# Kernel tuning notes

Measured on AMD Instinct MI355X. Metric: run time of the kernel, lower is better.

## Reference

```python
import jax, jax.numpy as jnp
import numpy as np

N_NODES = 100000
N_EDGES = 1600000
IN_DIM = 512
HID_DIM = 64
N_CLASSES = 10
N_GRAPHS = 64


def setup_inputs() -> dict:
    key = jax.random.key(0)
    ks = jax.random.split(key, 8)
    x = jax.random.normal(ks[0], (N_NODES, IN_DIM), dtype=jnp.float32)
    edge_src = jax.random.randint(ks[1], (N_EDGES,), 0, N_NODES)
    edge_dst = jax.random.randint(ks[2], (N_EDGES,), 0, N_NODES)
    node2graph = jnp.sort(jax.random.randint(ks[3], (N_NODES,), 0, N_GRAPHS))
    W1 = jax.random.normal(ks[4], (IN_DIM, HID_DIM), dtype=jnp.float32) * (1.0 / np.sqrt(IN_DIM))
    b1 = jnp.zeros((HID_DIM,), dtype=jnp.float32)
    W2 = jax.random.normal(ks[5], (HID_DIM, N_CLASSES), dtype=jnp.float32) * (1.0 / np.sqrt(HID_DIM))
    b2 = jnp.zeros((N_CLASSES,), dtype=jnp.float32)
    return {"x": x, "edge_src": edge_src, "edge_dst": edge_dst,
            "node2graph": node2graph, "n_graphs": N_GRAPHS,
            "W1": W1, "b1": b1, "W2": W2, "b2": b2}


def reference(x, edge_src, edge_dst, node2graph, n_graphs, W1, b1, W2, b2):
    n = x.shape[0]
    ones_e = jnp.ones(edge_src.shape[0], dtype=x.dtype)
    # DGL GraphConv norm='both': src scaled by out-deg^-1/2, dst by in-deg^-1/2 (degrees clamped to 1)
    out_deg = jax.ops.segment_sum(ones_e, edge_src, num_segments=n)
    in_deg = jax.ops.segment_sum(ones_e, edge_dst, num_segments=n)
    src_norm = jax.lax.rsqrt(jnp.maximum(out_deg, 1.0))  # [N]
    dst_norm = jax.lax.rsqrt(jnp.maximum(in_deg, 1.0))   # [N]

    def graph_conv(h, W, b):
        h = (h * src_norm[:, None]) @ W                       # [N, out]
        agg = jax.ops.segment_sum(h[edge_src], edge_dst, num_segments=n)  # SpMM
        return agg * dst_norm[:, None] + b

    h = jax.nn.relu(graph_conv(x, W1, b1))
    h = graph_conv(h, W2, b2)
    # dgl.mean_nodes: per-graph mean over nodes
    counts = jax.ops.segment_sum(jnp.ones(n, dtype=x.dtype), node2graph, num_segments=n_graphs)
    sums = jax.ops.segment_sum(h, node2graph, num_segments=n_graphs)
    return sums / jnp.maximum(counts, 1.0)[:, None]
```

## Files before the change

kernel.cpp:

```cpp
#include <hip/hip_runtime.h>

#define NN 100000
#define NE 1600000
#define NG 64
#define BPB  50
#define NBUK 2000
#define NBUK2 2048
#define ECAP 1120
#define GPART 256
#define NSLICE 8
#define SLB (GPART/NSLICE)
#define PREPB 128
#define ZEROB 3
#define GSTB ((NN+255)/256)

using bf16x8 = __attribute__((ext_vector_type(8))) short;
using f32x4  = __attribute__((ext_vector_type(4))) float;

__device__ inline unsigned short f2bf(float f){
    union { float f; unsigned u; } v; v.f = f;
    unsigned r = (v.u + 0x7FFFu + ((v.u >> 16) & 1u)) >> 16;
    return (unsigned short)r;
}

__device__ inline bf16x8 cvt8(float4 a, float4 b){
    union { unsigned u[4]; bf16x8 v; } r;
    asm("v_cvt_pk_bf16_f32 %0, %1, %2" : "=v"(r.u[0]) : "v"(a.x), "v"(a.y));
    asm("v_cvt_pk_bf16_f32 %0, %1, %2" : "=v"(r.u[1]) : "v"(a.z), "v"(a.w));
    asm("v_cvt_pk_bf16_f32 %0, %1, %2" : "=v"(r.u[2]) : "v"(b.x), "v"(b.y));
    asm("v_cvt_pk_bf16_f32 %0, %1, %2" : "=v"(r.u[3]) : "v"(b.z), "v"(b.w));
    return r.v;
}

__global__ __launch_bounds__(256) void k_start(const int* __restrict__ src, const int* __restrict__ dst,
                                               int* __restrict__ cntD, int* __restrict__ cntS, int E,
                                               const float* __restrict__ W1, short* __restrict__ Wb,
                                               float* __restrict__ pooled,
                                               const int* __restrict__ n2g, int* __restrict__ gstart, int N){
    __shared__ int hD[NBUK2], hS[NBUK2];
    int bid = blockIdx.x;
    int tid = threadIdx.x;
    if (bid < GPART){
        for (int i=tid; i<NBUK2; i+=256){ hD[i]=0; hS[i]=0; }
        __syncthreads();
        int chunk = (E + GPART - 1)/GPART;
        int start = bid*chunk;
        int end   = min(E, start + chunk);
        for (int e = start + tid; e < end; e += 256){
            atomicAdd(&hS[src[e]/BPB], 1);
            atomicAdd(&hD[dst[e]/BPB], 1);
        }
        __syncthreads();
        for (int i=tid; i<NBUK2; i+=256){
            cntD[bid*NBUK2 + i] = hD[i];
            cntS[bid*NBUK2 + i] = hS[i];
        }
    } else if (bid < GPART+PREPB){
        int i = (bid-GPART)*256 + tid;
        if (i < 512*64){
            int k = i >> 6, c = i & 63;
            int g = k >> 5, r = k & 31, s = r >> 3, j = r & 7;
            Wb[(((g*4+s)*64 + c) << 3) + j] = (short)f2bf(W1[i]);
        }
    } else if (bid < GPART+PREPB+ZEROB){
        int i = (bid-GPART-PREPB)*256 + tid;
        if (i < NG*10) pooled[i] = 0.f;
    } else {
        int n = (bid-GPART-PREPB-ZEROB)*256 + tid;
        if (n < N){
            int g  = n2g[n];
            int gp = (n == 0) ? -1 : n2g[n-1];
            if (gp != g){
                for (int gg = gp+1; gg <= g; ++gg) gstart[gg] = n;
            }
            if (n == N-1){
                for (int gg = g+1; gg <= NG; ++gg) gstart[gg] = N;
            }
        }
    }
}

__global__ __launch_bounds__(256) void k_scanCa(const int* __restrict__ cntD, const int* __restrict__ cntS,
                                                int* __restrict__ sliceD, int* __restrict__ sliceS){
    int id = blockIdx.x*256 + threadIdx.x;
    int t = id & (NBUK2-1);
    int s = id >> 11;
    int b0 = s*SLB;
    int sD=0, sS=0;
    for (int b=b0; b<b0+SLB; b++){ sD += cntD[b*NBUK2+t]; sS += cntS[b*NBUK2+t]; }
    sliceD[s*NBUK2+t] = sD;
    sliceS[s*NBUK2+t] = sS;
}

__global__ __launch_bounds__(1024) void k_scanB(const int* __restrict__ sliceD, const int* __restrict__ sliceS,
                                                int* __restrict__ bstartD, int* __restrict__ bstartS){
    __shared__ int sd[1024];
    int t = threadIdx.x;
    {
        int v0=0, v1=0;
        #pragma unroll
        for (int s=0;s<NSLICE;s++){ v0 += sliceD[s*NBUK2 + 2*t]; v1 += sliceD[s*NBUK2 + 2*t+1]; }
        sd[t] = v0+v1; __syncthreads();
        for (int off=1; off<1024; off<<=1){
            int tv = (t >= off) ? sd[t-off] : 0;
            __syncthreads();
            sd[t] += tv;
            __syncthreads();
        }
        int excl = sd[t] - v0 - v1;
        if (2*t   <= NBUK) bstartD[2*t]   = excl;
        if (2*t+1 <= NBUK) bstartD[2*t+1] = excl + v0;
        __syncthreads();
    }
    {
        int v0=0, v1=0;
        #pragma unroll
        for (int s=0;s<NSLICE;s++){ v0 += sliceS[s*NBUK2 + 2*t]; v1 += sliceS[s*NBUK2 + 2*t+1]; }
        sd[t] = v0+v1; __syncthreads();
        for (int off=1; off<1024; off<<=1){
            int tv = (t >= off) ? sd[t-off] : 0;
            __syncthreads();
            sd[t] += tv;
            __syncthreads();
        }
        int excl = sd[t] - v0 - v1;
        if (2*t   <= NBUK) bstartS[2*t]   = excl;
        if (2*t+1 <= NBUK) bstartS[2*t+1] = excl + v0;
    }
}

__global__ __launch_bounds__(256) void k_scanCb(int* __restrict__ cntD, int* __restrict__ cntS,
                                                const int* __restrict__ sliceD, const int* __restrict__ sliceS,
                                                const int* __restrict__ bstartD, const int* __restrict__ bstartS){
    int id = blockIdx.x*256 + threadIdx.x;
    int t = id & (NBUK2-1);
    int s = id >> 11;
    if (t >= NBUK) return;
    int rD = bstartD[t], rS = bstartS[t];
    for (int sp=0; sp<s; sp++){ rD += sliceD[sp*NBUK2+t]; rS += sliceS[sp*NBUK2+t]; }
    int b0 = s*SLB;
    for (int b=b0; b<b0+SLB; b++){
        int idx = b*NBUK2 + t;
        int o = cntD[idx]; cntD[idx] = rD; rD += o;
        o = cntS[idx];     cntS[idx] = rS; rS += o;
    }
}

__global__ __launch_bounds__(256) void k_scatter(const int* __restrict__ src, const int* __restrict__ dst,
                                                 const int* __restrict__ cntD, const int* __restrict__ cntS,
                                                 int* __restrict__ pairs, unsigned char* __restrict__ srcb, int E){
    __shared__ unsigned oD[NBUK2], oS[NBUK2];
    for (int i=threadIdx.x; i<NBUK2; i+=256){
        oD[i] = (unsigned)cntD[blockIdx.x*NBUK2 + i];
        oS[i] = (unsigned)cntS[blockIdx.x*NBUK2 + i];
    }
    __syncthreads();
    int chunk = (E + GPART - 1)/GPART;
    int start = blockIdx.x*chunk;
    int end   = min(E, start + chunk);
    for (int e = start + threadIdx.x; e < end; e += 256){
        int s = src[e], d = dst[e];
        int bk = d/BPB;
        unsigned pD = atomicAdd(&oD[bk], 1u);
        pairs[pD] = (s << 6) | (d - bk*BPB);
        int sb = s/BPB;
        unsigned pS = atomicAdd(&oS[sb], 1u);
        srcb[pS] = (unsigned char)(s - sb*BPB);
    }
}

__global__ __launch_bounds__(256) void k_outdeg(const unsigned char* __restrict__ srcb,
                                                const int* __restrict__ bstartS,
                                                float* __restrict__ sn, int N){
    __shared__ int c[BPB];
    int b = blockIdx.x;
    if (threadIdx.x < BPB) c[threadIdx.x] = 0;
    __syncthreads();
    int s0 = bstartS[b], s1 = bstartS[b+1];
    for (int i = s0 + threadIdx.x; i < s1; i += 256)
        atomicAdd(&c[srcb[i]], 1);
    __syncthreads();
    int node = b*BPB + threadIdx.x;
    if (threadIdx.x < BPB && node < N)
        sn[node] = rsqrtf((float)max(c[threadIdx.x], 1));
}

__global__ __launch_bounds__(256) void k_gemm1(const float* __restrict__ x, const short* __restrict__ Wb,
                                               const float* __restrict__ sn, unsigned short* __restrict__ hb, int N){
    const int lane = threadIdx.x & 63;
    const int wid  = threadIdx.x >> 6;
    const int rowBase = blockIdx.x*128 + wid*32;
    const int mrow = lane & 15;
    const int s    = lane >> 4;

    int rowA = rowBase + mrow;
    int rowB = rowBase + 16 + mrow;
    int rcA = (rowA < N) ? rowA : (N-1);
    int rcB = (rowB < N) ? rowB : (N-1);

    const float4* __restrict__ xv = (const float4*)x;
    const bf16x8* __restrict__ wv = (const bf16x8*)Wb;
    const float4* xrA = xv + (size_t)rcA*128 + s*2;
    const float4* xrB = xv + (size_t)rcB*128 + s*2;

    f32x4 accA0 = {0,0,0,0}, accA1 = {0,0,0,0}, accA2 = {0,0,0,0}, accA3 = {0,0,0,0};
    f32x4 accB0 = {0,0,0,0}, accB1 = {0,0,0,0}, accB2 = {0,0,0,0}, accB3 = {0,0,0,0};

    #pragma unroll 2
    for (int g=0; g<16; g++){
        float4 a0 = xrA[g*8 + 0];
        float4 a1 = xrA[g*8 + 1];
        float4 c0 = xrB[g*8 + 0];
        float4 c1 = xrB[g*8 + 1];
        bf16x8 afA = cvt8(a0, a1);
        bf16x8 afB = cvt8(c0, c1);
        int bbase = (g*4 + s)*64 + mrow;
        bf16x8 b0 = wv[bbase     ];
        bf16x8 b1 = wv[bbase + 16];
        bf16x8 b2 = wv[bbase + 32];
        bf16x8 b3 = wv[bbase + 48];
        accA0 = __builtin_amdgcn_mfma_f32_16x16x32_bf16(afA, b0, accA0, 0, 0, 0);
        accA1 = __builtin_amdgcn_mfma_f32_16x16x32_bf16(afA, b1, accA1, 0, 0, 0);
        accA2 = __builtin_amdgcn_mfma_f32_16x16x32_bf16(afA, b2, accA2, 0, 0, 0);
        accA3 = __builtin_amdgcn_mfma_f32_16x16x32_bf16(afA, b3, accA3, 0, 0, 0);
        accB0 = __builtin_amdgcn_mfma_f32_16x16x32_bf16(afB, b0, accB0, 0, 0, 0);
        accB1 = __builtin_amdgcn_mfma_f32_16x16x32_bf16(afB, b1, accB1, 0, 0, 0);
        accB2 = __builtin_amdgcn_mfma_f32_16x16x32_bf16(afB, b2, accB2, 0, 0, 0);
        accB3 = __builtin_amdgcn_mfma_f32_16x16x32_bf16(afB, b3, accB3, 0, 0, 0);
    }

    #pragma unroll
    for (int q=0; q<4; q++){
        int rr = rowBase + s*4 + q;
        if (rr < N){
            float scale = sn[rr];
            unsigned short* hp = hb + ((size_t)rr<<6) + mrow;
            hp[ 0] = f2bf(accA0[q] * scale);
            hp[16] = f2bf(accA1[q] * scale);
            hp[32] = f2bf(accA2[q] * scale);
            hp[48] = f2bf(accA3[q] * scale);
        }
        int r2 = rowBase + 16 + s*4 + q;
        if (r2 < N){
            float scale = sn[r2];
            unsigned short* hp = hb + ((size_t)r2<<6) + mrow;
            hp[ 0] = f2bf(accB0[q] * scale);
            hp[16] = f2bf(accB1[q] * scale);
            hp[32] = f2bf(accB2[q] * scale);
            hp[48] = f2bf(accB3[q] * scale);
        }
    }
}

__global__ __launch_bounds__(256) void k_agg(const int* __restrict__ pairs, const int* __restrict__ bstartD,
                                             const unsigned short* __restrict__ hb,
                                             const float* __restrict__ sn, const float* __restrict__ b1,
                                             const float* __restrict__ W2,
                                             float* __restrict__ h2, int* __restrict__ gsrc,
                                             int* __restrict__ glh, int N){
    __shared__ int lsrc[ECAP];
    __shared__ int lcnt[BPB];
    __shared__ int lstart[BPB+1];
    __shared__ unsigned lofs[BPB];
    __shared__ __align__(16) float w2t[10][64];
    __shared__ float b1s[64];
    __shared__ __align__(16) float a1s[BPB][68];
    int tid = threadIdx.x;
    if (tid < BPB) lcnt[tid] = 0;
    if (tid < 64)  b1s[tid] = b1[tid];
    for (int i=tid; i<640; i+=256){ int c = i>>6, k = i&63; w2t[c][k] = W2[k*10 + c]; }
    __syncthreads();

    int b = blockIdx.x;
    int nodeBase = b*BPB;
    int eb = bstartD[b], ee = bstartD[b+1];
    int ne = ee - eb;

    for (int i = tid; i < ne; i += 256){
        int pr = pairs[eb + i];
        atomicAdd(&lcnt[pr & 63], 1);
    }
    __syncthreads();
    if (tid < 64){
        int v = (tid < BPB) ? lcnt[tid] : 0;
        int sI = v;
        for (int off=1; off<64; off<<=1){
            int t = __shfl_up(sI, off);
            if (tid >= off) sI += t;
        }
        if (tid < BPB){
            lstart[tid] = sI - v;
            lofs[tid]   = (unsigned)(sI - v);
            if (tid == BPB-1) lstart[BPB] = sI;
        }
    }
    __syncthreads();
    for (int i = tid; i < ne; i += 256){
        int pr = pairs[eb + i];
        unsigned pos = atomicAdd(&lofs[pr & 63], 1u);
        lsrc[pos < ECAP ? pos : ECAP-1] = pr >> 6;
    }
    __syncthreads();

    for (int i = tid; i < ne; i += 256) gsrc[eb + i] = lsrc[i];
    if (tid <= BPB) glh[b*64 + tid] = eb + lstart[tid];

    int lane = tid & 63, wid = tid >> 6;
    int q  = lane >> 4;
    int c4 = lane & 15;

    for (int nl = wid; nl < BPB; nl += 4){
        int node = nodeBase + nl;
        int s0 = lstart[nl];
        int m  = lstart[nl+1] - s0;

        float a0=0.f, a1f=0.f, a2=0.f, a3=0.f;
        int j = 0;
        for (; j + 16 <= m; j += 16){
            int sa = lsrc[s0 + j + q];
            int sb = lsrc[s0 + j + 4 + q];
            int sc = lsrc[s0 + j + 8 + q];
            int sd = lsrc[s0 + j + 12 + q];
            uint2 va = *(const uint2*)(hb + ((size_t)sa<<6) + (c4<<2));
            uint2 vb = *(const uint2*)(hb + ((size_t)sb<<6) + (c4<<2));
            uint2 vc = *(const uint2*)(hb + ((size_t)sc<<6) + (c4<<2));
            uint2 vd = *(const uint2*)(hb + ((size_t)sd<<6) + (c4<<2));
            a0  += __uint_as_float((va.x & 0xffffu) << 16) + __uint_as_float((vb.x & 0xffffu) << 16)
                 + __uint_as_float((vc.x & 0xffffu) << 16) + __uint_as_float((vd.x & 0xffffu) << 16);
            a1f += __uint_as_float(va.x & 0xffff0000u) + __uint_as_float(vb.x & 0xffff0000u)
                 + __uint_as_float(vc.x & 0xffff0000u) + __uint_as_float(vd.x & 0xffff0000u);
            a2  += __uint_as_float((va.y & 0xffffu) << 16) + __uint_as_float((vb.y & 0xffffu) << 16)
                 + __uint_as_float((vc.y & 0xffffu) << 16) + __uint_as_float((vd.y & 0xffffu) << 16);
            a3  += __uint_as_float(va.y & 0xffff0000u) + __uint_as_float(vb.y & 0xffff0000u)
                 + __uint_as_float(vc.y & 0xffff0000u) + __uint_as_float(vd.y & 0xffff0000u);
        }
        for (; j + 8 <= m; j += 8){
            int sa = lsrc[s0 + j + q];
            int sb = lsrc[s0 + j + 4 + q];
            uint2 va = *(const uint2*)(hb + ((size_t)sa<<6) + (c4<<2));
            uint2 vb = *(const uint2*)(hb + ((size_t)sb<<6) + (c4<<2));
            a0  += __uint_as_float((va.x & 0xffffu) << 16) + __uint_as_float((vb.x & 0xffffu) << 16);
            a1f += __uint_as_float(va.x & 0xffff0000u) + __uint_as_float(vb.x & 0xffff0000u);
            a2  += __uint_as_float((va.y & 0xffffu) << 16) + __uint_as_float((vb.y & 0xffffu) << 16);
            a3  += __uint_as_float(va.y & 0xffff0000u) + __uint_as_float(vb.y & 0xffff0000u);
        }
        for (; j < m; j += 4){
            int idx = j + q;
            int idxc = (idx < m) ? idx : (m-1);
            int sa = lsrc[s0 + idxc];
            uint2 va = *(const uint2*)(hb + ((size_t)sa<<6) + (c4<<2));
            if (idx < m){
                a0  += __uint_as_float((va.x & 0xffffu) << 16);
                a1f += __uint_as_float(va.x & 0xffff0000u);
                a2  += __uint_as_float((va.y & 0xffffu) << 16);
                a3  += __uint_as_float(va.y & 0xffff0000u);
            }
        }
        a0  += __shfl_xor(a0, 16);  a0  += __shfl_xor(a0, 32);
        a1f += __shfl_xor(a1f, 16); a1f += __shfl_xor(a1f, 32);
        a2  += __shfl_xor(a2, 16);  a2  += __shfl_xor(a2, 32);
        a3  += __shfl_xor(a3, 16);  a3  += __shfl_xor(a3, 32);

        float dnv = rsqrtf((float)max(m, 1));
        float snv = sn[node];
        float r0 = fmaxf(fmaf(a0,  dnv, b1s[(c4<<2)+0]), 0.f) * snv;
        float r1 = fmaxf(fmaf(a1f, dnv, b1s[(c4<<2)+1]), 0.f) * snv;
        float r2 = fmaxf(fmaf(a2,  dnv, b1s[(c4<<2)+2]), 0.f) * snv;
        float r3 = fmaxf(fmaf(a3,  dnv, b1s[(c4<<2)+3]), 0.f) * snv;
        if (q == 0){
            *(float4*)(&a1s[nl][c4<<2]) = make_float4(r0, r1, r2, r3);
        }
    }
    __syncthreads();

    for (int i = tid; i < BPB*10; i += 256){
        int nl = i / 10;
        int c  = i - nl*10;
        int node = nodeBase + nl;
        if (node < N){
            const float4* ap = (const float4*)(&a1s[nl][0]);
            const float4* wp = (const float4*)(&w2t[c][0]);
            float acc = 0.f;
            #pragma unroll
            for (int p=0;p<16;p++){
                float4 a = ap[p]; float4 w = wp[p];
                acc = fmaf(a.x, w.x, fmaf(a.y, w.y, fmaf(a.z, w.z, fmaf(a.w, w.w, acc))));
            }
            h2[(size_t)node*16 + c] = acc;
        }
    }
}

__global__ __launch_bounds__(256) void k_pool2(const int* __restrict__ gsrc, const int* __restrict__ glh,
                                               const float* __restrict__ h2, const int* __restrict__ n2g,
                                               float* __restrict__ pooled, int N){
    __shared__ float accS[NG*10];
    int tid = threadIdx.x;
    for (int i=tid; i<NG*10; i+=256) accS[i] = 0.f;
    __syncthreads();
    int b = blockIdx.x;
    int nodeBase = b*BPB;
    int lane = tid & 63, wid = tid >> 6;
    int e6 = lane/10, c = lane - e6*10;
    bool active = (lane < 60);

    for (int nl = wid; nl < BPB; nl += 4){
        int node = nodeBase + nl;
        int base = glh[b*64 + nl];
        int m    = glh[b*64 + nl + 1] - base;
        float acc = 0.f;
        for (int j = 0; j < m; j += 6){
            int idx = j + e6;
            int idxc = (idx < m) ? idx : (m-1);
            int srcn = gsrc[base + idxc];
            float v = h2[(size_t)srcn*16 + c];
            if (active && idx < m) acc += v;
        }
        float t0 = __shfl(acc, lane+30); if (lane < 30) acc += t0;
        float t1 = __shfl(acc, lane+10);
        float t2 = __shfl(acc, lane+20);
        if (lane < 10){
            acc += t1 + t2;
            float dnv = rsqrtf((float)max(m, 1));
            int g = n2g[node];
            atomicAdd(&accS[g*10 + lane], dnv*acc);
        }
    }
    __syncthreads();
    int g0 = n2g[nodeBase], g1 = n2g[nodeBase + BPB - 1];
    int lo = g0*10, hi = g1*10 + 10;
    for (int i = lo + tid; i < hi; i += 256)
        atomicAdd(&pooled[i], accS[i]);
}

__global__ void k_out(const float* __restrict__ pooled, const int* __restrict__ gstart,
                      const float* __restrict__ b2, float* __restrict__ out){
    int i = blockIdx.x*blockDim.x + threadIdx.x;
    if (i < NG*10){
        int g = i/10, c = i - g*10;
        float cnt = (float)max(gstart[g+1] - gstart[g], 1);
        out[i] = pooled[i]/cnt + b2[c];
    }
}

extern "C" void kernel_launch(void* const* d_in, const int* in_sizes, int n_in,
                              void* d_out, int out_size, void* d_ws, size_t ws_size,
                              hipStream_t stream) {
    const float* x    = (const float*)d_in[0];
    const int*   esrc = (const int*)d_in[1];
    const int*   edst = (const int*)d_in[2];
    const int*   n2g  = (const int*)d_in[3];
    const float* W1   = (const float*)d_in[5];
    const float* b1   = (const float*)d_in[6];
    const float* W2   = (const float*)d_in[7];
    const float* b2   = (const float*)d_in[8];
    float* out = (float*)d_out;
    const int N = in_sizes[3];
    const int E = in_sizes[1];

    char* ws = (char*)d_ws;
    size_t off = 0;
    auto alloc = [&](size_t bytes) -> void* {
        void* p = ws + off;
        off = (off + bytes + 255) & ~(size_t)255;
        return p;
    };
    float* pooled  = (float*)alloc(NG*10*4);
    int*   cntD    = (int*)alloc((size_t)GPART*NBUK2*4);
    int*   cntS    = (int*)alloc((size_t)GPART*NBUK2*4);
    int*   sliceD  = (int*)alloc((size_t)NSLICE*NBUK2*4);
    int*   sliceS  = (int*)alloc((size_t)NSLICE*NBUK2*4);
    int*   bstartD = (int*)alloc((NBUK+1)*4);
    int*   bstartS = (int*)alloc((NBUK+1)*4);
    int*   pairs   = (int*)alloc((size_t)E*4);
    unsigned char* srcb = (unsigned char*)alloc((size_t)E);
    int*   gsrc    = (int*)alloc((size_t)E*4);
    int*   glh     = (int*)alloc((size_t)NBUK*64*4);
    float* sn      = (float*)alloc((size_t)N*4);
    int*   gstart  = (int*)alloc((size_t)(NG+1)*4);
    short* Wb      = (short*)alloc((size_t)512*64*2);
    unsigned short* hb = (unsigned short*)alloc((size_t)N*64*2);
    float* h2      = (float*)alloc((size_t)N*16*4);

    k_start<<<dim3(GPART+PREPB+ZEROB+GSTB), dim3(256), 0, stream>>>(
        esrc, edst, cntD, cntS, E, W1, Wb, pooled, n2g, gstart, N);
    k_scanCa<<<dim3(64), dim3(256), 0, stream>>>(cntD, cntS, sliceD, sliceS);
    k_scanB<<<dim3(1), dim3(1024), 0, stream>>>(sliceD, sliceS, bstartD, bstartS);
    k_scanCb<<<dim3(64), dim3(256), 0, stream>>>(cntD, cntS, sliceD, sliceS, bstartD, bstartS);
    k_scatter<<<dim3(GPART), dim3(256), 0, stream>>>(esrc, edst, cntD, cntS, pairs, srcb, E);
    k_outdeg<<<dim3(NBUK), dim3(256), 0, stream>>>(srcb, bstartS, sn, N);

    k_gemm1<<<dim3((N+127)/128), dim3(256), 0, stream>>>(x, Wb, sn, hb, N);

    k_agg<<<dim3(NBUK), dim3(256), 0, stream>>>(pairs, bstartD, hb, sn, b1, W2, h2, gsrc, glh, N);
    k_pool2<<<dim3(NBUK), dim3(256), 0, stream>>>(gsrc, glh, h2, n2g, pooled, N);
    k_out<<<dim3(3), dim3(256), 0, stream>>>(pooled, gstart, b2, out);
}
```

Measured before the change: 231.3 us.

## Pad per-node edge lists to multiples of four with a zero sentinel node

Each node's local edge list in k_agg is rounded up to a multiple of four and filled with a sentinel index N, which points at zeroed padding rows appended to hb and h2. This removes the bounds-checked tail loops in the aggregation. gsrc becomes a fixed per-bucket layout whose offsets and true counts are packed into glh. The histogram and scatter passes now load edges as int4 vectors. The cost is extra gather traffic on padded entries and a slightly larger ECAP, and the int4 path assumes E is a multiple of four.

```diff
diff --git a/kernel.cpp b/kernel.cpp
--- a/kernel.cpp
+++ b/kernel.cpp
@@ -6,7 +6,7 @@
 #define BPB  50
 #define NBUK 2000
 #define NBUK2 2048
-#define ECAP 1120
+#define ECAP 1152
 #define GPART 256
 #define NSLICE 8
 #define SLB (GPART/NSLICE)
@@ -36,6 +36,7 @@
                                                int* __restrict__ cntD, int* __restrict__ cntS, int E,
                                                const float* __restrict__ W1, short* __restrict__ Wb,
                                                float* __restrict__ pooled,
+                                               unsigned short* __restrict__ hb, float* __restrict__ h2,
                                                const int* __restrict__ n2g, int* __restrict__ gstart, int N){
     __shared__ int hD[NBUK2], hS[NBUK2];
     int bid = blockIdx.x;
@@ -43,12 +44,16 @@
     if (bid < GPART){
         for (int i=tid; i<NBUK2; i+=256){ hD[i]=0; hS[i]=0; }
         __syncthreads();
-        int chunk = (E + GPART - 1)/GPART;
-        int start = bid*chunk;
-        int end   = min(E, start + chunk);
-        for (int e = start + tid; e < end; e += 256){
-            atomicAdd(&hS[src[e]/BPB], 1);
-            atomicAdd(&hD[dst[e]/BPB], 1);
+        int EV = E >> 2;
+        int chunkV = (EV + GPART - 1)/GPART;
+        int sV = bid*chunkV, eV = min(EV, sV+chunkV);
+        for (int v = sV + tid; v < eV; v += 256){
+            int4 s4 = ((const int4*)src)[v];
+            int4 d4 = ((const int4*)dst)[v];
+            atomicAdd(&hS[s4.x/BPB], 1); atomicAdd(&hS[s4.y/BPB], 1);
+            atomicAdd(&hS[s4.z/BPB], 1); atomicAdd(&hS[s4.w/BPB], 1);
+            atomicAdd(&hD[d4.x/BPB], 1); atomicAdd(&hD[d4.y/BPB], 1);
+            atomicAdd(&hD[d4.z/BPB], 1); atomicAdd(&hD[d4.w/BPB], 1);
         }
         __syncthreads();
         for (int i=tid; i<NBUK2; i+=256){
@@ -65,6 +70,8 @@
     } else if (bid < GPART+PREPB+ZEROB){
         int i = (bid-GPART-PREPB)*256 + tid;
         if (i < NG*10) pooled[i] = 0.f;
+        else if (i < NG*10 + 64) hb[(size_t)N*64 + (i - NG*10)] = 0;
+        else if (i < NG*10 + 64 + 16) h2[(size_t)N*16 + (i - NG*10 - 64)] = 0.f;
     } else {
         int n = (bid-GPART-PREPB-ZEROB)*256 + tid;
         if (n < N){
@@ -155,17 +162,23 @@
         oS[i] = (unsigned)cntS[blockIdx.x*NBUK2 + i];
     }
     __syncthreads();
-    int chunk = (E + GPART - 1)/GPART;
-    int start = blockIdx.x*chunk;
-    int end   = min(E, start + chunk);
-    for (int e = start + threadIdx.x; e < end; e += 256){
-        int s = src[e], d = dst[e];
-        int bk = d/BPB;
-        unsigned pD = atomicAdd(&oD[bk], 1u);
-        pairs[pD] = (s << 6) | (d - bk*BPB);
-        int sb = s/BPB;
-        unsigned pS = atomicAdd(&oS[sb], 1u);
-        srcb[pS] = (unsigned char)(s - sb*BPB);
+    int EV = E >> 2;
+    int chunkV = (EV + GPART - 1)/GPART;
+    int sV = blockIdx.x*chunkV, eV = min(EV, sV+chunkV);
+    for (int v = sV + threadIdx.x; v < eV; v += 256){
+        int4 s4 = ((const int4*)src)[v];
+        int4 d4 = ((const int4*)dst)[v];
+        #pragma unroll
+        for (int k=0;k<4;k++){
+            int s = (k==0)?s4.x:(k==1)?s4.y:(k==2)?s4.z:s4.w;
+            int d = (k==0)?d4.x:(k==1)?d4.y:(k==2)?d4.z:d4.w;
+            int bk = d/BPB;
+            unsigned pD = atomicAdd(&oD[bk], 1u);
+            pairs[pD] = (s << 6) | (d - bk*BPB);
+            int sb = s/BPB;
+            unsigned pS = atomicAdd(&oS[sb], 1u);
+            srcb[pS] = (unsigned char)(s - sb*BPB);
+        }
     }
 }
 
@@ -268,6 +281,7 @@
     int tid = threadIdx.x;
     if (tid < BPB) lcnt[tid] = 0;
     if (tid < 64)  b1s[tid] = b1[tid];
+    for (int i=tid; i<ECAP; i+=256) lsrc[i] = N;
     for (int i=tid; i<640; i+=256){ int c = i>>6, k = i&63; w2t[c][k] = W2[k*10 + c]; }
     __syncthreads();
 
@@ -282,7 +296,8 @@
     }
     __syncthreads();
     if (tid < 64){
-        int v = (tid < BPB) ? lcnt[tid] : 0;
+        int mt = (tid < BPB) ? lcnt[tid] : 0;
+        int v = (mt + 3) & ~3;
         int sI = v;
         for (int off=1; off<64; off<<=1){
             int t = __shfl_up(sI, off);
@@ -302,8 +317,12 @@
     }
     __syncthreads();
 
-    for (int i = tid; i < ne; i += 256) gsrc[eb + i] = lsrc[i];
-    if (tid <= BPB) glh[b*64 + tid] = eb + lstart[tid];
+    int ptot = lstart[BPB];
+    for (int i = tid; i < ptot; i += 256) gsrc[b*ECAP + i] = lsrc[i];
+    if (tid <= BPB){
+        int mt = (tid < BPB) ? lcnt[tid] : 0;
+        glh[b*64 + tid] = (lstart[tid] & 0xFFFF) | (mt << 16);
+    }
 
     int lane = tid & 63, wid = tid >> 6;
     int q  = lane >> 4;
@@ -312,11 +331,12 @@
     for (int nl = wid; nl < BPB; nl += 4){
         int node = nodeBase + nl;
         int s0 = lstart[nl];
-        int m  = lstart[nl+1] - s0;
+        int m4 = lstart[nl+1] - s0;
+        int mt = lcnt[nl];
 
         float a0=0.f, a1f=0.f, a2=0.f, a3=0.f;
         int j = 0;
-        for (; j + 16 <= m; j += 16){
+        for (; j + 16 <= m4; j += 16){
             int sa = lsrc[s0 + j + q];
             int sb = lsrc[s0 + j + 4 + q];
             int sc = lsrc[s0 + j + 8 + q];
@@ -334,34 +354,20 @@
             a3  += __uint_as_float(va.y & 0xffff0000u) + __uint_as_float(vb.y & 0xffff0000u)
                  + __uint_as_float(vc.y & 0xffff0000u) + __uint_as_float(vd.y & 0xffff0000u);
         }
-        for (; j + 8 <= m; j += 8){
+        for (; j < m4; j += 4){
             int sa = lsrc[s0 + j + q];
-            int sb = lsrc[s0 + j + 4 + q];
             uint2 va = *(const uint2*)(hb + ((size_t)sa<<6) + (c4<<2));
-            uint2 vb = *(const uint2*)(hb + ((size_t)sb<<6) + (c4<<2));
-            a0  += __uint_as_float((va.x & 0xffffu) << 16) + __uint_as_float((vb.x & 0xffffu) << 16);
-            a1f += __uint_as_float(va.x & 0xffff0000u) + __uint_as_float(vb.x & 0xffff0000u);
-            a2  += __uint_as_float((va.y & 0xffffu) << 16) + __uint_as_float((vb.y & 0xffffu) << 16);
-            a3  += __uint_as_float(va.y & 0xffff0000u) + __uint_as_float(vb.y & 0xffff0000u);
-        }
-        for (; j < m; j += 4){
-            int idx = j + q;
-            int idxc = (idx < m) ? idx : (m-1);
-            int sa = lsrc[s0 + idxc];
-            uint2 va = *(const uint2*)(hb + ((size_t)sa<<6) + (c4<<2));
-            if (idx < m){
-                a0  += __uint_as_float((va.x & 0xffffu) << 16);
-                a1f += __uint_as_float(va.x & 0xffff0000u);
-                a2  += __uint_as_float((va.y & 0xffffu) << 16);
-                a3  += __uint_as_float(va.y & 0xffff0000u);
-            }
+            a0  += __uint_as_float((va.x & 0xffffu) << 16);
+            a1f += __uint_as_float(va.x & 0xffff0000u);
+            a2  += __uint_as_float((va.y & 0xffffu) << 16);
+            a3  += __uint_as_float(va.y & 0xffff0000u);
         }
         a0  += __shfl_xor(a0, 16);  a0  += __shfl_xor(a0, 32);
         a1f += __shfl_xor(a1f, 16); a1f += __shfl_xor(a1f, 32);
         a2  += __shfl_xor(a2, 16);  a2  += __shfl_xor(a2, 32);
         a3  += __shfl_xor(a3, 16);  a3  += __shfl_xor(a3, 32);
 
-        float dnv = rsqrtf((float)max(m, 1));
+        float dnv = rsqrtf((float)max(mt, 1));
         float snv = sn[node];
         float r0 = fmaxf(fmaf(a0,  dnv, b1s[(c4<<2)+0]), 0.f) * snv;
         float r1 = fmaxf(fmaf(a1f, dnv, b1s[(c4<<2)+1]), 0.f) * snv;
@@ -406,22 +412,25 @@
 
     for (int nl = wid; nl < BPB; nl += 4){
         int node = nodeBase + nl;
-        int base = glh[b*64 + nl];
-        int m    = glh[b*64 + nl + 1] - base;
+        int cur = glh[b*64 + nl];
+        int nxt = glh[b*64 + nl + 1];
+        int base = b*ECAP + (cur & 0xFFFF);
+        int m4   = (nxt & 0xFFFF) - (cur & 0xFFFF);
+        int mt   = cur >> 16;
         float acc = 0.f;
-        for (int j = 0; j < m; j += 6){
+        for (int j = 0; j < m4; j += 6){
             int idx = j + e6;
-            int idxc = (idx < m) ? idx : (m-1);
+            int idxc = (idx < m4) ? idx : (m4-1);
             int srcn = gsrc[base + idxc];
             float v = h2[(size_t)srcn*16 + c];
-            if (active && idx < m) acc += v;
+            if (active && idx < m4) acc += v;
         }
         float t0 = __shfl(acc, lane+30); if (lane < 30) acc += t0;
         float t1 = __shfl(acc, lane+10);
         float t2 = __shfl(acc, lane+20);
         if (lane < 10){
             acc += t1 + t2;
-            float dnv = rsqrtf((float)max(m, 1));
+            float dnv = rsqrtf((float)max(mt, 1));
             int g = n2g[node];
             atomicAdd(&accS[g*10 + lane], dnv*acc);
         }
@@ -474,16 +483,16 @@
     int*   bstartS = (int*)alloc((NBUK+1)*4);
     int*   pairs   = (int*)alloc((size_t)E*4);
     unsigned char* srcb = (unsigned char*)alloc((size_t)E);
-    int*   gsrc    = (int*)alloc((size_t)E*4);
+    int*   gsrc    = (int*)alloc((size_t)NBUK*ECAP*4);
     int*   glh     = (int*)alloc((size_t)NBUK*64*4);
     float* sn      = (float*)alloc((size_t)N*4);
     int*   gstart  = (int*)alloc((size_t)(NG+1)*4);
     short* Wb      = (short*)alloc((size_t)512*64*2);
-    unsigned short* hb = (unsigned short*)alloc((size_t)N*64*2);
-    float* h2      = (float*)alloc((size_t)N*16*4);
+    unsigned short* hb = (unsigned short*)alloc((size_t)(N+1)*64*2);
+    float* h2      = (float*)alloc((size_t)(N+1)*16*4);
 
     k_start<<<dim3(GPART+PREPB+ZEROB+GSTB), dim3(256), 0, stream>>>(
-        esrc, edst, cntD, cntS, E, W1, Wb, pooled, n2g, gstart, N);
+        esrc, edst, cntD, cntS, E, W1, Wb, pooled, hb, h2, n2g, gstart, N);
     k_scanCa<<<dim3(64), dim3(256), 0, stream>>>(cntD, cntS, sliceD, sliceS);
     k_scanB<<<dim3(1), dim3(1024), 0, stream>>>(sliceD, sliceS, bstartD, bstartS);
     k_scanCb<<<dim3(64), dim3(256), 0, stream>>>(cntD, cntS, sliceD, sliceS, bstartD, bstartS);
```

Measured after the change: 218.6 us. 1.06x faster.
